# Kernel tuning notes

Measured on AMD Instinct MI355X. Metric: run time of the kernel, lower is better.

Reference implementation:

```python
import jax, jax.numpy as jnp
import numpy as np

H = 50  # hidden_dim
L = 4   # num_layers

def setup_inputs() -> dict:
    key = jax.random.key(0)
    ks = jax.random.split(key, 12)
    B, T, D = 2048, 512, 1
    s0 = 1.0 / np.sqrt(H)  # PyTorch GRU init scale
    x = jax.random.normal(ks[0], (B, T, D), dtype=jnp.float32)
    # layer 0 (input size 1)
    W_ih0 = jax.random.uniform(ks[1], (3 * H, D), minval=-s0, maxval=s0, dtype=jnp.float32)
    W_hh0 = jax.random.uniform(ks[2], (3 * H, H), minval=-s0, maxval=s0, dtype=jnp.float32)
    b_ih0 = jax.random.uniform(ks[3], (3 * H,), minval=-s0, maxval=s0, dtype=jnp.float32)
    b_hh0 = jax.random.uniform(ks[4], (3 * H,), minval=-s0, maxval=s0, dtype=jnp.float32)
    # layers 1..3 stacked (input size H)
    W_ih = jax.random.uniform(ks[5], (L - 1, 3 * H, H), minval=-s0, maxval=s0, dtype=jnp.float32)
    W_hh = jax.random.uniform(ks[6], (L - 1, 3 * H, H), minval=-s0, maxval=s0, dtype=jnp.float32)
    b_ih = jax.random.uniform(ks[7], (L - 1, 3 * H), minval=-s0, maxval=s0, dtype=jnp.float32)
    b_hh = jax.random.uniform(ks[8], (L - 1, 3 * H), minval=-s0, maxval=s0, dtype=jnp.float32)
    fc_w = jax.random.uniform(ks[9], (1, H), minval=-s0, maxval=s0, dtype=jnp.float32)
    fc_b = jax.random.uniform(ks[10], (1,), minval=-s0, maxval=s0, dtype=jnp.float32)
    return {"x": x, "W_ih0": W_ih0, "W_hh0": W_hh0, "b_ih0": b_ih0, "b_hh0": b_hh0,
            "W_ih": W_ih, "W_hh": W_hh, "b_ih": b_ih, "b_hh": b_hh,
            "fc_w": fc_w, "fc_b": fc_b}


def _gru_layer(x_seq, Wih, Whh, bih, bhh):
    # x_seq: [B, T, Din] -> outputs [B, T, H]. PyTorch GRU cell math.
    gx = jnp.einsum('btd,gd->btg', x_seq, Wih) + bih  # [B, T, 3H], precomputed input gates
    gx = jnp.transpose(gx, (1, 0, 2))  # [T, B, 3H]
    h0 = jnp.zeros((x_seq.shape[0], H), dtype=x_seq.dtype)

    def step(h, gxt):
        gh = h @ Whh.T + bhh  # [B, 3H]
        xr, xz, xn = jnp.split(gxt, 3, axis=-1)
        hr, hz, hn = jnp.split(gh, 3, axis=-1)
        r = jax.nn.sigmoid(xr + hr)
        z = jax.nn.sigmoid(xz + hz)
        n = jnp.tanh(xn + r * hn)
        h_new = (1.0 - z) * n + z * h
        return h_new, h_new

    _, hs = jax.lax.scan(step, h0, gx)  # hs: [T, B, H]
    return jnp.transpose(hs, (1, 0, 2))  # [B, T, H]


def reference(x, W_ih0, W_hh0, b_ih0, b_hh0, W_ih, W_hh, b_ih, b_hh, fc_w, fc_b):
    out = _gru_layer(x, W_ih0, W_hh0, b_ih0, b_hh0)
    for l in range(L - 1):  # eval mode: dropout inactive
        out = _gru_layer(out, W_ih[l], W_hh[l], b_ih[l], b_hh[l])
    last = out[:, -1, :]  # [B, H]
    logits = last @ fc_w.T + fc_b  # [B, 1]
    return jax.nn.sigmoid(logits)
```

## Files before the change

### kernel.cpp

```cpp
#include <hip/hip_runtime.h>
#include <hip/hip_fp16.h>

#define HDIM  50
#define G3    150
#define TSEQ  512
#define BATCH 2048
#define NBC   16
#define NLAY  4

typedef _Float16 f16x8 __attribute__((ext_vector_type(8)));
typedef float    f32x4 __attribute__((ext_vector_type(4)));

#define MFMA(a,b,c) __builtin_amdgcn_mfma_f32_16x16x32_f16((a),(b),(c),0,0,0)

static __device__ inline unsigned pk2(float a, float b) {
    return __builtin_bit_cast(unsigned, __builtin_amdgcn_cvt_pkrtz(a, b));
}
static __device__ inline float rcpf(float x) { return __builtin_amdgcn_rcpf(x); }

#if __has_builtin(__builtin_amdgcn_exp2f)
static __device__ inline float ex2(float x) { return __builtin_amdgcn_exp2f(x); }
#else
static __device__ inline float ex2(float x) {
    float r; asm volatile("v_exp_f32 %0, %1" : "=v"(r) : "v"(x)); return r;
}
#endif

#define SCL_RZ (-1.44269504f)
#define SCL_N  ( 2.88539008f)

__global__ __launch_bounds__(512, 2)
void gru_8w(const float* __restrict__ xin,
            const float* __restrict__ Wih0, const float* __restrict__ Whh0,
            const float* __restrict__ bih0, const float* __restrict__ bhh0,
            const float* __restrict__ WihL, const float* __restrict__ WhhL,
            const float* __restrict__ bihL, const float* __restrict__ bhhL,
            const float* __restrict__ fcw,  const float* __restrict__ fcb,
            float* __restrict__ out)
{
    const int tid  = threadIdx.x;
    const int wid  = tid >> 6;
    const int lay  = wid >> 1;
    const int wm   = wid & 1;
    const int lane = tid & 63;
    const int lb   = lane & 15;
    const int lg   = lane >> 4;
    const int b0   = (blockIdx.x & 127) * NBC;
    const bool wr  = (blockIdx.x < 128);

    __shared__ __align__(16) _Float16 hsl[NLAY][2][16][72];
    __shared__ float x_row[NBC][516];

    const float* Wih = (lay==0) ? Wih0 : WihL + (size_t)(lay-1)*G3*HDIM;
    const float* Whh = (lay==0) ? Whh0 : WhhL + (size_t)(lay-1)*G3*HDIM;
    const float* bih = (lay==0) ? bih0 : bihL + (lay-1)*G3;
    const float* bhh = (lay==0) ? bhh0 : bhhL + (lay-1)*G3;

    f16x8 a_hh[3][2][2], a_ih[3][2][2];
#pragma unroll
    for (int g = 0; g < 3; ++g) {
#pragma unroll
        for (int sub = 0; sub < 2; ++sub) {
            const int  ur = (2*wm + sub)*16 + lb;
            const bool rv = ur < HDIM;
            const int  gr = 50*g + (rv ? ur : 0);
            const float scl = (g < 2) ? SCL_RZ : SCL_N;
#pragma unroll
            for (int kt = 0; kt < 2; ++kt) {
                f16x8 fh, fi;
#pragma unroll
                for (int j = 0; j < 8; ++j) {
                    const int k = 32*kt + 8*lg + j;
                    float vh = 0.f, vi = 0.f;
                    if (rv) {
                        if (k < HDIM)       vh = Whh[gr*HDIM + k];
                        else if (k == HDIM) vh = bhh[gr];
                        if (lay == 0) {
                            if (kt == 0 && k == 0)      vi = Wih[gr];
                            else if (kt == 0 && k == 1) vi = bih[gr];
                        } else {
                            if (k < HDIM)       vi = Wih[gr*HDIM + k];
                            else if (k == HDIM) vi = bih[gr];
                        }
                    }
                    fh[j] = (_Float16)(vh * scl); fi[j] = (_Float16)(vi * scl);
                }
                a_hh[g][sub][kt] = fh; a_ih[g][sub][kt] = fi;
            }
        }
    }

    for (int k = tid; k < NBC*TSEQ; k += 512)
        x_row[k >> 9][k & 511] = xin[(size_t)(b0 + (k >> 9))*TSEQ + (k & 511)];
    for (int k = tid; k < NLAY*2*16*72; k += 512)
        ((_Float16*)hsl)[k] = (_Float16)(((k % 72) == HDIM) ? 1.f : 0.f);

    float hold[2][4];
#pragma unroll
    for (int sub = 0; sub < 2; ++sub)
#pragma unroll
        for (int i = 0; i < 4; ++i) hold[sub][i] = 0.f;
    __syncthreads();

    f16x8 bh0 = *(const f16x8*)&hsl[lay][1][lb][8*lg];
    f16x8 bh1 = *(const f16x8*)&hsl[lay][1][lb][32 + 8*lg];
    f16x8 bx0{}, bx1{};
    if (lay == 0) {
#pragma unroll
        for (int j = 0; j < 8; ++j) bx0[j] = (_Float16)0.f;
        if (lg == 0) { bx0[0] = (_Float16)x_row[lb][0]; bx0[1] = (_Float16)1.f; }
    } else {
        bx0 = *(const f16x8*)&hsl[lay-1][1][lb][8*lg];
        bx1 = *(const f16x8*)&hsl[lay-1][1][lb][32 + 8*lg];
    }
    const f32x4 Z4 = {0.f, 0.f, 0.f, 0.f};

    for (int s = 0; s < TSEQ + NLAY - 1; ++s) {
        const int t = s - lay;
        if (t >= 0 && t < TSEQ) {
            f32x4 acc[3][2], accx[2];
#pragma unroll
            for (int g = 0; g < 3; ++g)
#pragma unroll
                for (int sub = 0; sub < 2; ++sub)
                    acc[g][sub] = MFMA(a_hh[g][sub][0], bh0, Z4);
#pragma unroll
            for (int g = 0; g < 3; ++g)
#pragma unroll
                for (int sub = 0; sub < 2; ++sub)
                    acc[g][sub] = MFMA(a_hh[g][sub][1], bh1, acc[g][sub]);
#pragma unroll
            for (int g = 0; g < 2; ++g)
#pragma unroll
                for (int sub = 0; sub < 2; ++sub)
                    acc[g][sub] = MFMA(a_ih[g][sub][0], bx0, acc[g][sub]);
#pragma unroll
            for (int sub = 0; sub < 2; ++sub)
                accx[sub] = MFMA(a_ih[2][sub][0], bx0, Z4);
            if (lay != 0) {
#pragma unroll
                for (int g = 0; g < 2; ++g)
#pragma unroll
                    for (int sub = 0; sub < 2; ++sub)
                        acc[g][sub] = MFMA(a_ih[g][sub][1], bx1, acc[g][sub]);
#pragma unroll
                for (int sub = 0; sub < 2; ++sub)
                    accx[sub] = MFMA(a_ih[2][sub][1], bx1, accx[sub]);
            }

#pragma unroll
            for (int g = 0; g < 2; ++g)
#pragma unroll
                for (int sub = 0; sub < 2; ++sub)
#pragma unroll
                    for (int i = 0; i < 4; ++i) {
                        if (wm == 1 && sub == 1 && i >= 2) continue;
                        acc[g][sub][i] = rcpf(1.f + ex2(acc[g][sub][i]));
                    }

            float hp[2][4];
#pragma unroll
            for (int sub = 0; sub < 2; ++sub)
#pragma unroll
                for (int i = 0; i < 4; ++i) {
                    if (wm == 1 && sub == 1 && i >= 2) { hp[sub][i] = 0.f; continue; }
                    const float r  = acc[0][sub][i];
                    const float z  = acc[1][sub][i];
                    const float vp = accx[sub][i] + r * acc[2][sub][i];
                    const float n  = 1.f - 2.f*rcpf(ex2(vp) + 1.f);
                    const float h  = fmaf(z, hold[sub][i] - n, n);
                    hold[sub][i] = h;
                    hp[sub][i] = h;
                }

            {
                _Float16* hrow = &hsl[lay][s & 1][lb][0];
#pragma unroll
                for (int sub = 0; sub < 2; ++sub) {
                    if (wm == 1 && sub == 1) {
                        if (lg == 0)
                            *(unsigned*)&hrow[48] = pk2(hp[1][0], hp[1][1]);
                    } else {
                        uint2 q; q.x = pk2(hp[sub][0], hp[sub][1]);
                                 q.y = pk2(hp[sub][2], hp[sub][3]);
                        *(uint2*)&hrow[16*(2*wm + sub) + 4*lg] = q;
                    }
                }
            }
        }
        __syncthreads();

        const int pb = s & 1;
        bh0 = *(const f16x8*)&hsl[lay][pb][lb][8*lg];
        bh1 = *(const f16x8*)&hsl[lay][pb][lb][32 + 8*lg];
        if (lay == 0) {
            const int tt = (s+1 < TSEQ) ? s+1 : TSEQ-1;
            if (lg == 0) bx0[0] = (_Float16)x_row[lb][tt];
        } else {
            bx0 = *(const f16x8*)&hsl[lay-1][pb][lb][8*lg];
            bx1 = *(const f16x8*)&hsl[lay-1][pb][lb][32 + 8*lg];
        }
    }

    if (wr && tid < NBC) {
        float sacc = fcb[0];
#pragma unroll
        for (int j = 0; j < HDIM; ++j)
            sacc = fmaf((float)hsl[NLAY-1][0][tid][j], fcw[j], sacc);
        out[b0 + tid] = rcpf(1.f + __expf(-sacc));
    }
}

extern "C" void kernel_launch(void* const* d_in, const int* in_sizes, int n_in,
                              void* d_out, int out_size, void* d_ws, size_t ws_size,
                              hipStream_t stream) {
    const float* x     = (const float*)d_in[0];
    const float* W_ih0 = (const float*)d_in[1];
    const float* W_hh0 = (const float*)d_in[2];
    const float* b_ih0 = (const float*)d_in[3];
    const float* b_hh0 = (const float*)d_in[4];
    const float* W_ih  = (const float*)d_in[5];
    const float* W_hh  = (const float*)d_in[6];
    const float* b_ih  = (const float*)d_in[7];
    const float* b_hh  = (const float*)d_in[8];
    const float* fc_w  = (const float*)d_in[9];
    const float* fc_b  = (const float*)d_in[10];
    float* out = (float*)d_out;

    dim3 grid(256), block(512);
    gru_8w<<<grid, block, 0, stream>>>(
        x, W_ih0, W_hh0, b_ih0, b_hh0,
        W_ih, W_hh, b_ih, b_hh, fc_w, fc_b, out);
}
```

Measured before the change: 534.9 us.

## Split each GRU layer across four waves, one 16-row hidden tile each

Measured after the change: 545.4 us. No clear change (+2.0%).

```diff
diff --git a/kernel.cpp b/kernel.cpp
--- a/kernel.cpp
+++ b/kernel.cpp
@@ -29,19 +29,19 @@
 #define SCL_RZ (-1.44269504f)
 #define SCL_N  ( 2.88539008f)
 
-__global__ __launch_bounds__(512, 2)
-void gru_8w(const float* __restrict__ xin,
-            const float* __restrict__ Wih0, const float* __restrict__ Whh0,
-            const float* __restrict__ bih0, const float* __restrict__ bhh0,
-            const float* __restrict__ WihL, const float* __restrict__ WhhL,
-            const float* __restrict__ bihL, const float* __restrict__ bhhL,
-            const float* __restrict__ fcw,  const float* __restrict__ fcb,
-            float* __restrict__ out)
+__global__ __launch_bounds__(1024, 4)
+void gru_16w(const float* __restrict__ xin,
+             const float* __restrict__ Wih0, const float* __restrict__ Whh0,
+             const float* __restrict__ bih0, const float* __restrict__ bhh0,
+             const float* __restrict__ WihL, const float* __restrict__ WhhL,
+             const float* __restrict__ bihL, const float* __restrict__ bhhL,
+             const float* __restrict__ fcw,  const float* __restrict__ fcb,
+             float* __restrict__ out)
 {
     const int tid  = threadIdx.x;
     const int wid  = tid >> 6;
-    const int lay  = wid >> 1;
-    const int wm   = wid & 1;
+    const int lay  = wid >> 2;
+    const int wt   = wid & 3;
     const int lane = tid & 63;
     const int lb   = lane & 15;
     const int lg   = lane >> 4;
@@ -56,50 +56,45 @@
     const float* bih = (lay==0) ? bih0 : bihL + (lay-1)*G3;
     const float* bhh = (lay==0) ? bhh0 : bhhL + (lay-1)*G3;
 
-    f16x8 a_hh[3][2][2], a_ih[3][2][2];
+    const int  ur = 16*wt + lb;
+    const bool rv = ur < HDIM;
+    f16x8 a_hh[3][2], a_ih[3][2];
 #pragma unroll
     for (int g = 0; g < 3; ++g) {
-#pragma unroll
-        for (int sub = 0; sub < 2; ++sub) {
-            const int  ur = (2*wm + sub)*16 + lb;
-            const bool rv = ur < HDIM;
-            const int  gr = 50*g + (rv ? ur : 0);
-            const float scl = (g < 2) ? SCL_RZ : SCL_N;
-#pragma unroll
-            for (int kt = 0; kt < 2; ++kt) {
-                f16x8 fh, fi;
-#pragma unroll
-                for (int j = 0; j < 8; ++j) {
-                    const int k = 32*kt + 8*lg + j;
-                    float vh = 0.f, vi = 0.f;
-                    if (rv) {
-                        if (k < HDIM)       vh = Whh[gr*HDIM + k];
-                        else if (k == HDIM) vh = bhh[gr];
-                        if (lay == 0) {
-                            if (kt == 0 && k == 0)      vi = Wih[gr];
-                            else if (kt == 0 && k == 1) vi = bih[gr];
-                        } else {
-                            if (k < HDIM)       vi = Wih[gr*HDIM + k];
-                            else if (k == HDIM) vi = bih[gr];
-                        }
+        const int  gr  = 50*g + (rv ? ur : 0);
+        const float scl = (g < 2) ? SCL_RZ : SCL_N;
+#pragma unroll
+        for (int kt = 0; kt < 2; ++kt) {
+            f16x8 fh, fi;
+#pragma unroll
+            for (int j = 0; j < 8; ++j) {
+                const int k = 32*kt + 8*lg + j;
+                float vh = 0.f, vi = 0.f;
+                if (rv) {
+                    if (k < HDIM)       vh = Whh[gr*HDIM + k];
+                    else if (k == HDIM) vh = bhh[gr];
+                    if (lay == 0) {
+                        if (kt == 0 && k == 0)      vi = Wih[gr];
+                        else if (kt == 0 && k == 1) vi = bih[gr];
+                    } else {
+                        if (k < HDIM)       vi = Wih[gr*HDIM + k];
+                        else if (k == HDIM) vi = bih[gr];
                     }
-                    fh[j] = (_Float16)(vh * scl); fi[j] = (_Float16)(vi * scl);
                 }
-                a_hh[g][sub][kt] = fh; a_ih[g][sub][kt] = fi;
-            }
+                fh[j] = (_Float16)(vh * scl); fi[j] = (_Float16)(vi * scl);
+            }
+            a_hh[g][kt] = fh; a_ih[g][kt] = fi;
         }
     }
 
-    for (int k = tid; k < NBC*TSEQ; k += 512)
+    for (int k = tid; k < NBC*TSEQ; k += 1024)
         x_row[k >> 9][k & 511] = xin[(size_t)(b0 + (k >> 9))*TSEQ + (k & 511)];
-    for (int k = tid; k < NLAY*2*16*72; k += 512)
+    for (int k = tid; k < NLAY*2*16*72; k += 1024)
         ((_Float16*)hsl)[k] = (_Float16)(((k % 72) == HDIM) ? 1.f : 0.f);
 
-    float hold[2][4];
-#pragma unroll
-    for (int sub = 0; sub < 2; ++sub)
-#pragma unroll
-        for (int i = 0; i < 4; ++i) hold[sub][i] = 0.f;
+    float hold[4];
+#pragma unroll
+    for (int i = 0; i < 4; ++i) hold[i] = 0.f;
     __syncthreads();
 
     f16x8 bh0 = *(const f16x8*)&hsl[lay][1][lb][8*lg];
@@ -115,76 +110,54 @@
     }
     const f32x4 Z4 = {0.f, 0.f, 0.f, 0.f};
 
+    const bool t3 = (wt == 3);
+
     for (int s = 0; s < TSEQ + NLAY - 1; ++s) {
         const int t = s - lay;
         if (t >= 0 && t < TSEQ) {
-            f32x4 acc[3][2], accx[2];
-#pragma unroll
-            for (int g = 0; g < 3; ++g)
-#pragma unroll
-                for (int sub = 0; sub < 2; ++sub)
-                    acc[g][sub] = MFMA(a_hh[g][sub][0], bh0, Z4);
-#pragma unroll
-            for (int g = 0; g < 3; ++g)
-#pragma unroll
-                for (int sub = 0; sub < 2; ++sub)
-                    acc[g][sub] = MFMA(a_hh[g][sub][1], bh1, acc[g][sub]);
+            f32x4 acc[3], accx;
+#pragma unroll
+            for (int g = 0; g < 3; ++g) acc[g] = MFMA(a_hh[g][0], bh0, Z4);
+#pragma unroll
+            for (int g = 0; g < 3; ++g) acc[g] = MFMA(a_hh[g][1], bh1, acc[g]);
+#pragma unroll
+            for (int g = 0; g < 2; ++g) acc[g] = MFMA(a_ih[g][0], bx0, acc[g]);
+            accx = MFMA(a_ih[2][0], bx0, Z4);
+            if (lay != 0) {
+#pragma unroll
+                for (int g = 0; g < 2; ++g) acc[g] = MFMA(a_ih[g][1], bx1, acc[g]);
+                accx = MFMA(a_ih[2][1], bx1, accx);
+            }
+
 #pragma unroll
             for (int g = 0; g < 2; ++g)
 #pragma unroll
-                for (int sub = 0; sub < 2; ++sub)
-                    acc[g][sub] = MFMA(a_ih[g][sub][0], bx0, acc[g][sub]);
-#pragma unroll
-            for (int sub = 0; sub < 2; ++sub)
-                accx[sub] = MFMA(a_ih[2][sub][0], bx0, Z4);
-            if (lay != 0) {
-#pragma unroll
-                for (int g = 0; g < 2; ++g)
-#pragma unroll
-                    for (int sub = 0; sub < 2; ++sub)
-                        acc[g][sub] = MFMA(a_ih[g][sub][1], bx1, acc[g][sub]);
-#pragma unroll
-                for (int sub = 0; sub < 2; ++sub)
-                    accx[sub] = MFMA(a_ih[2][sub][1], bx1, accx[sub]);
-            }
-
-#pragma unroll
-            for (int g = 0; g < 2; ++g)
-#pragma unroll
-                for (int sub = 0; sub < 2; ++sub)
-#pragma unroll
-                    for (int i = 0; i < 4; ++i) {
-                        if (wm == 1 && sub == 1 && i >= 2) continue;
-                        acc[g][sub][i] = rcpf(1.f + ex2(acc[g][sub][i]));
-                    }
-
-            float hp[2][4];
-#pragma unroll
-            for (int sub = 0; sub < 2; ++sub)
-#pragma unroll
                 for (int i = 0; i < 4; ++i) {
-                    if (wm == 1 && sub == 1 && i >= 2) { hp[sub][i] = 0.f; continue; }
-                    const float r  = acc[0][sub][i];
-                    const float z  = acc[1][sub][i];
-                    const float vp = accx[sub][i] + r * acc[2][sub][i];
-                    const float n  = 1.f - 2.f*rcpf(ex2(vp) + 1.f);
-                    const float h  = fmaf(z, hold[sub][i] - n, n);
-                    hold[sub][i] = h;
-                    hp[sub][i] = h;
+                    if (t3 && i >= 2) continue;
+                    acc[g][i] = rcpf(1.f + ex2(acc[g][i]));
                 }
+
+            float hp[4];
+#pragma unroll
+            for (int i = 0; i < 4; ++i) {
+                if (t3 && i >= 2) { hp[i] = 0.f; continue; }
+                const float r  = acc[0][i];
+                const float z  = acc[1][i];
+                const float vp = accx[i] + r * acc[2][i];
+                const float n  = 1.f - 2.f*rcpf(ex2(vp) + 1.f);
+                const float h  = fmaf(z, hold[i] - n, n);
+                hold[i] = h;
+                hp[i] = h;
+            }
 
             {
                 _Float16* hrow = &hsl[lay][s & 1][lb][0];
-#pragma unroll
-                for (int sub = 0; sub < 2; ++sub) {
-                    if (wm == 1 && sub == 1) {
-                        if (lg == 0)
-                            *(unsigned*)&hrow[48] = pk2(hp[1][0], hp[1][1]);
-                    } else {
-                        uint2 q; q.x = pk2(hp[sub][0], hp[sub][1]);
-                                 q.y = pk2(hp[sub][2], hp[sub][3]);
-                        *(uint2*)&hrow[16*(2*wm + sub) + 4*lg] = q;
-                    }
+                if (!t3) {
+                    uint2 q; q.x = pk2(hp[0], hp[1]);
+                             q.y = pk2(hp[2], hp[3]);
+                    *(uint2*)&hrow[16*wt + 4*lg] = q;
+                } else if (lg == 0) {
+                    *(unsigned*)&hrow[48] = pk2(hp[0], hp[1]);
                 }
             }
         }
@@ -227,8 +200,8 @@
     const float* fc_b  = (const float*)d_in[10];
     float* out = (float*)d_out;
 
-    dim3 grid(256), block(512);
-    gru_8w<<<grid, block, 0, stream>>>(
+    dim3 grid(256), block(1024);
+    gru_16w<<<grid, block, 0, stream>>>(
         x, W_ih0, W_hh0, b_ih0, b_hh0,
         W_ih, W_hh, b_ih, b_hh, fc_w, fc_b, out);
 }
```
